# Kernel optimization log

Hardware: AMD Instinct MI355X
Metric: run time of the kernel (lower is better)

## Reference

```python
import jax, jax.numpy as jnp
import numpy as np


def setup_inputs() -> dict:
    key = jax.random.key(0)
    ks = jax.random.split(key, 8)
    N, D, E, R = 300000, 64, 1000000, 100000
    all_emb = jax.random.normal(ks[0], (N, D), jnp.float32)
    # xavier-ish init for the edge MLP (Linear(2D->D), Linear(D->1))
    W1 = jax.random.normal(ks[1], (D, 2 * D), jnp.float32) / np.sqrt(2.0 * D).astype(np.float32)
    b1 = jnp.zeros((D,), jnp.float32)
    W2 = jax.random.normal(ks[2], (1, D), jnp.float32) / np.sqrt(1.0 * D).astype(np.float32)
    b2 = jnp.zeros((1,), jnp.float32)
    edge_index = jax.random.randint(ks[3], (2, E), 0, N, jnp.int32)
    rand_idx = jax.random.randint(ks[4], (2, R), 0, N, jnp.int32)
    eps_u = jax.random.uniform(ks[5], (E, 1), jnp.float32)
    rb_u = jax.random.uniform(ks[6], (E,), jnp.float32)
    return dict(all_emb=all_emb, W1=W1, b1=b1, W2=W2, b2=b2,
                edge_index=edge_index, rand_idx=rand_idx, eps_u=eps_u, rb_u=rb_u)


def reference(all_emb, W1, b1, W2, b2, edge_index, rand_idx, eps_u, rb_u):
    src, dst = edge_index[0], edge_index[1]
    # gather + concat: [E, 2D]
    edge_emb = jnp.concatenate([all_emb[src], all_emb[dst]], axis=1)
    h = jax.nn.relu(edge_emb @ W1.T + b1)            # [E, D]
    edge_logits = h @ W2.T + b2                      # [E, 1]
    # Gumbel-sigmoid gate, temperature 1.0; eps ~ U(bias, 1-bias)
    bias = 1e-4
    eps = (bias - (1.0 - bias)) * eps_u + (1.0 - bias)
    gate = jnp.log(eps) - jnp.log1p(-eps) + edge_logits
    edge_weight = jax.nn.sigmoid(gate)[:, 0]         # [E]
    # __build_prob_neighbourhood: RelaxedBernoulli(temp=0.9, probs=clamp(w,.01,.99)).rsample()
    att = jnp.clip(edge_weight, 0.01, 0.99)
    u = jnp.clip(rb_u, 1e-7, 1.0 - 1e-7)
    t = 0.9
    sample = jax.nn.sigmoid((jnp.log(att) - jnp.log1p(-att) + jnp.log(u) - jnp.log1p(-u)) / t)
    mask = jax.lax.stop_gradient((sample > 0.0).astype(sample.dtype))
    mat = sample * mask
    # sparse rebuild: (edge_index, mat) + graph_random (rand_idx, 0.05), then coalesce
    rand_vals = jnp.full((rand_idx.shape[1],), 0.05, mat.dtype)
    rows = jnp.concatenate([src, rand_idx[0]])
    cols = jnp.concatenate([dst, rand_idx[1]])
    vals = jnp.concatenate([mat, rand_vals])
    order = jnp.lexsort((cols, rows))                # sort by (row, col)
    rows_s, cols_s, vals_s = rows[order], cols[order], vals[order]
    change = jnp.concatenate([jnp.ones((1,), bool),
                              (rows_s[1:] != rows_s[:-1]) | (cols_s[1:] != cols_s[:-1])])
    seg = jnp.cumsum(change) - 1                     # run id per sorted entry
    sums = jax.ops.segment_sum(vals_s, seg, num_segments=vals.shape[0])
    # coalesced value placed at first occurrence of each unique (row,col); dups zeroed
    out_vals = jnp.where(change, sums[seg], 0.0)
    return rows_s, cols_s, out_vals
```

## Files before the change

kernel.cpp:

```cpp
#include <hip/hip_runtime.h>
#include <stdint.h>

typedef unsigned short u16;
typedef unsigned int   u32;
typedef __attribute__((ext_vector_type(8))) short bf16x8;
typedef __attribute__((ext_vector_type(4))) float f32x4;

#define RSTRIDE 32

__device__ __forceinline__ float bflo(u32 u){ return __uint_as_float(u << 16); }
__device__ __forceinline__ u32 f2bf(float f){
  u32 u = __float_as_uint(f);
  return (u + 0x7fffu + ((u >> 16) & 1u)) >> 16;
}
__device__ __forceinline__ float qbf(float f){ return __uint_as_float(f2bf(f) << 16); }
__device__ __forceinline__ float decp(u32 p){
  u32 lo = p & 8191u;
  return __uint_as_float((lo ? lo + 8192u : 0u) << 16);
}

__global__ void k_zero(int* __restrict__ c, int N){
  int i = blockIdx.x * 256 + threadIdx.x;
  if (i < N) c[i] = 0;
}

__global__ void __launch_bounds__(256) k_mlp_fused(
    const u16* __restrict__ emb, const u16* __restrict__ W1,
    const u16* __restrict__ b1, const u16* __restrict__ W2,
    const u16* __restrict__ b2,
    const int* __restrict__ src, const int* __restrict__ dst,
    const u16* __restrict__ eps_u, const u16* __restrict__ rb_u,
    const int* __restrict__ rand0, const int* __restrict__ rand1,
    int* __restrict__ cnt, u32* __restrict__ packed,
    int E, int R, int ntp)
{
  int lane = threadIdx.x & 63;
  int c    = lane & 15;
  int quad = lane >> 4;
  int wid  = blockIdx.x * 4 + (threadIdx.x >> 6);
  int wstride = gridDim.x * 4;

  {
    int gtid = blockIdx.x * 256 + threadIdx.x;
    int gsz  = gridDim.x * 256;
    for (int i = gtid; i < R; i += gsz){
      int row = rand0[i];
      int rk = atomicAdd(&cnt[row], 1);
      if (rk < RSTRIDE)
        packed[(size_t)row * RSTRIDE + rk] = ((u32)rand1[i] << 13) | 7501u;
    }
  }

  bf16x8 bfr[4][4];
  #pragma unroll
  for (int ks = 0; ks < 4; ks++)
    #pragma unroll
    for (int t = 0; t < 4; t++)
      bfr[ks][t] = *(const bf16x8*)(W1 + (size_t)(t*16 + c)*128 + ks*32 + quad*8);

  float b1v[4], w2v[4];
  #pragma unroll
  for (int t = 0; t < 4; t++){
    b1v[t] = bflo((u32)b1[t*16 + c]);
    w2v[t] = bflo((u32)W2[t*16 + c]);
  }
  float b2v = bflo((u32)b2[0]);

  int nd = 0;
  if (wid < ntp){
    int idx = wid * 32 + (lane & 31);
    if (idx >= E) idx = E - 1;
    nd = (lane < 32) ? src[idx] : dst[idx];
  }

  for (int tp = wid; tp < ntp; tp += wstride){
    int e_base = tp * 32;

    int tpn = tp + wstride;
    int ndn = 0;
    if (tpn < ntp){
      int idxn = tpn * 32 + (lane & 31);
      if (idxn >= E) idxn = E - 1;
      ndn = (lane < 32) ? src[idxn] : dst[idxn];
    }

    int s0 = __shfl(nd, c),      d0 = __shfl(nd, 32 + c);
    int s1 = __shfl(nd, 16 + c), d1 = __shfl(nd, 48 + c);

    int tile = c >> 2, r = c & 3;
    int eo32 = tile * 16 + quad * 4 + r;
    int e_o  = e_base + eo32;
    bool act = (c < 8) && (e_o < E);
    int s_e = __shfl(nd, eo32);
    int d_e = __shfl(nd, 32 + eo32);

    int rk = 0;
    if (act) rk = atomicAdd(&cnt[s_e], 1);

    bf16x8 a0[4], a1[4];
    #pragma unroll
    for (int ks = 0; ks < 4; ks++){
      a0[ks] = *(const bf16x8*)(emb + (size_t)(ks < 2 ? s0 : d0) * 64 + (ks & 1) * 32 + quad * 8);
      a1[ks] = *(const bf16x8*)(emb + (size_t)(ks < 2 ? s1 : d1) * 64 + (ks & 1) * 32 + quad * 8);
    }

    float ue = 0.f, uu_raw = 0.f;
    if (act){
      ue     = bflo((u32)eps_u[e_o]);
      uu_raw = bflo((u32)rb_u[e_o]);
    }

    f32x4 acc0[4], acc1[4];
    #pragma unroll
    for (int t = 0; t < 4; t++){
      acc0[t] = (f32x4){0.f,0.f,0.f,0.f};
      acc1[t] = (f32x4){0.f,0.f,0.f,0.f};
    }
    #pragma unroll
    for (int ks = 0; ks < 4; ks++){
      #pragma unroll
      for (int t = 0; t < 4; t++){
        acc0[t] = __builtin_amdgcn_mfma_f32_16x16x32_bf16(a0[ks], bfr[ks][t], acc0[t], 0, 0, 0);
        acc1[t] = __builtin_amdgcn_mfma_f32_16x16x32_bf16(a1[ks], bfr[ks][t], acc1[t], 0, 0, 0);
      }
    }

    float pr0[4], pr1[4];
    #pragma unroll
    for (int rr = 0; rr < 4; rr++){
      float h0 = fmaxf(acc0[0][rr] + b1v[0], 0.f);
      float h1 = fmaxf(acc0[1][rr] + b1v[1], 0.f);
      float h2 = fmaxf(acc0[2][rr] + b1v[2], 0.f);
      float h3 = fmaxf(acc0[3][rr] + b1v[3], 0.f);
      pr0[rr] = h0*w2v[0] + h1*w2v[1] + h2*w2v[2] + h3*w2v[3];
      float g0 = fmaxf(acc1[0][rr] + b1v[0], 0.f);
      float g1 = fmaxf(acc1[1][rr] + b1v[1], 0.f);
      float g2 = fmaxf(acc1[2][rr] + b1v[2], 0.f);
      float g3 = fmaxf(acc1[3][rr] + b1v[3], 0.f);
      pr1[rr] = g0*w2v[0] + g1*w2v[1] + g2*w2v[2] + g3*w2v[3];
    }
    #pragma unroll
    for (int d = 1; d < 16; d <<= 1){
      #pragma unroll
      for (int rr = 0; rr < 4; rr++){
        pr0[rr] += __shfl_xor(pr0[rr], d);
        pr1[rr] += __shfl_xor(pr1[rr], d);
      }
    }

    if (act){
      float pv0 = (r==0)?pr0[0]:(r==1)?pr0[1]:(r==2)?pr0[2]:pr0[3];
      float pv1 = (r==0)?pr1[0]:(r==1)?pr1[1]:(r==2)?pr1[2]:pr1[3];
      float logit = (tile ? pv1 : pv0) + b2v;
      float eps = fmaf(-0.9998f, ue, 0.9999f);
      float gate = (__log2f(eps) - __log2f(1.0f - eps)) * 0.69314718f + logit;
      gate = fminf(fmaxf(gate, -4.59511985f), 4.59511985f);
      float uu = fminf(fmaxf(uu_raw, 1e-7f), 1.0f - 1e-7f);
      float lu = (__log2f(uu) - __log2f(1.0f - uu)) * 0.69314718f;
      float l  = (gate + lu) * (1.0f / 0.9f);
      float ee = __builtin_amdgcn_exp2f(-l * 1.44269504f);
      float val = 1.0f / (1.0f + ee);
      u32 h = f2bf(val);
      u32 code = (h >= 8192u) ? (h - 8192u) : 0u;
      if (rk < RSTRIDE)
        packed[(size_t)s_e * RSTRIDE + rk] = ((u32)d_e << 13) | code;
    }

    nd = ndn;
  }
}

__global__ void k_scan1(const int* __restrict__ cnt, int* __restrict__ rowstart,
                        int* __restrict__ bsum, int N){
  __shared__ int sh[256];
  int blk = blockIdx.x, tid = threadIdx.x;
  int base = blk * 1024 + tid * 4;
  int v0 = (base + 0 < N) ? min(cnt[base + 0], RSTRIDE) : 0;
  int v1 = (base + 1 < N) ? min(cnt[base + 1], RSTRIDE) : 0;
  int v2 = (base + 2 < N) ? min(cnt[base + 2], RSTRIDE) : 0;
  int v3 = (base + 3 < N) ? min(cnt[base + 3], RSTRIDE) : 0;
  int tot = v0 + v1 + v2 + v3;
  sh[tid] = tot;
  __syncthreads();
  for (int off = 1; off < 256; off <<= 1){
    int t2 = (tid >= off) ? sh[tid - off] : 0;
    __syncthreads();
    sh[tid] += t2;
    __syncthreads();
  }
  int excl = sh[tid] - tot;
  if (base + 0 < N) rowstart[base + 0] = excl;
  if (base + 1 < N) rowstart[base + 1] = excl + v0;
  if (base + 2 < N) rowstart[base + 2] = excl + v0 + v1;
  if (base + 3 < N) rowstart[base + 3] = excl + v0 + v1 + v2;
  if (tid == 255) bsum[blk] = sh[255];
}

__global__ void k_scan2(const int* __restrict__ bsum, int* __restrict__ boff, int NB){
  __shared__ int sh[512];
  int tid = threadIdx.x;
  int v = (tid < NB) ? bsum[tid] : 0;
  sh[tid] = v;
  __syncthreads();
  for (int off = 1; off < 512; off <<= 1){
    int t2 = (tid >= off) ? sh[tid - off] : 0;
    __syncthreads();
    sh[tid] += t2;
    __syncthreads();
  }
  boff[tid] = sh[tid] - v;
}

#define CAS(a,b) { u32 x = v[a], y = v[b]; v[a] = min(x,y); v[b] = max(x,y); }

__global__ void __launch_bounds__(256) k_emit(
    const int* __restrict__ rowstart, const int* __restrict__ boff,
    const int* __restrict__ cnt, u32* __restrict__ packed,
    float* __restrict__ out, int N, int M){
  int r = blockIdx.x * 256 + threadIdx.x;
  if (r >= N) return;
  int deg = min(cnt[r], RSTRIDE);
  int b = rowstart[r] + boff[r >> 10];
  float rf = qbf((float)r);

  if (deg <= 16){
    const uint4* seg4 = (const uint4*)(packed + (size_t)r * RSTRIDE);
    uint4 q0 = seg4[0], q1 = seg4[1], q2 = seg4[2], q3 = seg4[3];
    u32 v[16];
    v[0]=q0.x; v[1]=q0.y; v[2]=q0.z; v[3]=q0.w;
    v[4]=q1.x; v[5]=q1.y; v[6]=q1.z; v[7]=q1.w;
    v[8]=q2.x; v[9]=q2.y; v[10]=q2.z; v[11]=q2.w;
    v[12]=q3.x; v[13]=q3.y; v[14]=q3.z; v[15]=q3.w;
    #pragma unroll
    for (int i = 0; i < 16; i++) if (i >= deg) v[i] = 0xFFFFFFFFu;

    CAS(0,1) CAS(2,3) CAS(4,5) CAS(6,7) CAS(8,9) CAS(10,11) CAS(12,13) CAS(14,15)
    CAS(0,2) CAS(1,3) CAS(4,6) CAS(5,7) CAS(8,10) CAS(9,11) CAS(12,14) CAS(13,15)
    CAS(1,2) CAS(5,6) CAS(9,10) CAS(13,14)
    CAS(0,4) CAS(1,5) CAS(2,6) CAS(3,7) CAS(8,12) CAS(9,13) CAS(10,14) CAS(11,15)
    CAS(2,4) CAS(3,5) CAS(10,12) CAS(11,13)
    CAS(1,2) CAS(3,4) CAS(5,6) CAS(9,10) CAS(11,12) CAS(13,14)
    CAS(0,8) CAS(1,9) CAS(2,10) CAS(3,11) CAS(4,12) CAS(5,13) CAS(6,14) CAS(7,15)
    CAS(4,8) CAS(5,9) CAS(6,10) CAS(7,11)
    CAS(2,4) CAS(3,5) CAS(6,8) CAS(7,9) CAS(10,12) CAS(11,13)
    CAS(1,2) CAS(3,4) CAS(5,6) CAS(7,8) CAS(9,10) CAS(11,12) CAS(13,14)

    #pragma unroll
    for (int i = 0; i < 16; i++){
      if (i < deg){
        u32 coli = v[i] >> 13;
        bool head = (i == 0) || ((v[i-1] >> 13) != coli);
        float s = decp(v[i]);
        bool run = true;
        #pragma unroll
        for (int j = i + 1; j < 16; j++){
          run = run && (j < deg) && ((v[j] >> 13) == coli);
          if (run) s += decp(v[j]);
        }
        float cf = qbf((float)coli);
        out[b + i]         = rf;
        out[M + b + i]     = cf;
        out[2 * M + b + i] = head ? qbf(s) : 0.f;
      }
    }
    return;
  }

  u32* seg = packed + (size_t)r * RSTRIDE;
  for (int i = 1; i < deg; i++){
    u32 p = seg[i];
    int j = i - 1;
    while (j >= 0 && seg[j] > p){ seg[j+1] = seg[j]; j--; }
    seg[j+1] = p;
  }
  int i = 0;
  while (i < deg){
    u32 p = seg[i];
    u32 col = p >> 13;
    float sum = decp(p);
    int j = i + 1;
    while (j < deg && (seg[j] >> 13) == col){
      sum += decp(seg[j]);
      j++;
    }
    float cf = qbf((float)col);
    out[b + i] = rf; out[M + b + i] = cf; out[2 * M + b + i] = qbf(sum);
    for (int q = i + 1; q < j; q++){
      out[b + q] = rf; out[M + b + q] = cf; out[2 * M + b + q] = 0.f;
    }
    i = j;
  }
}

extern "C" void kernel_launch(void* const* d_in, const int* in_sizes, int n_in,
                              void* d_out, int out_size, void* d_ws, size_t ws_size,
                              hipStream_t stream){
  (void)n_in; (void)out_size; (void)ws_size;
  const u16* all_emb = (const u16*)d_in[0];
  const u16* W1   = (const u16*)d_in[1];
  const u16* b1   = (const u16*)d_in[2];
  const u16* W2   = (const u16*)d_in[3];
  const u16* b2   = (const u16*)d_in[4];
  const int* edge_index = (const int*)d_in[5];
  const int* rand_idx   = (const int*)d_in[6];
  const u16* eps_u = (const u16*)d_in[7];
  const u16* rb_u  = (const u16*)d_in[8];

  int N = in_sizes[0] / 64;
  int E = in_sizes[5] / 2;
  int R = in_sizes[6] / 2;
  int M = E + R;
  const int* src   = edge_index;
  const int* dst   = edge_index + E;
  const int* rand0 = rand_idx;
  const int* rand1 = rand_idx + R;

  int* cnt      = (int*)d_ws;
  int* rowstart = cnt + N;
  int* bsum     = rowstart + N;
  int* boff     = bsum + 512;
  u32* packed   = (u32*)(boff + 512);

  k_zero<<<(N + 255) / 256, 256, 0, stream>>>(cnt, N);
  int ntp = (E + 31) / 32;
  k_mlp_fused<<<2048, 256, 0, stream>>>(all_emb, W1, b1, W2, b2, src, dst,
                                        eps_u, rb_u, rand0, rand1,
                                        cnt, packed, E, R, ntp);
  int NB = (N + 1023) / 1024;
  k_scan1<<<NB, 256, 0, stream>>>(cnt, rowstart, bsum, N);
  k_scan2<<<1, 512, 0, stream>>>(bsum, boff, NB);
  k_emit<<<(N + 255) / 256, 256, 0, stream>>>(rowstart, boff, cnt, packed,
                                              (float*)d_out, N, M);
}
```

Before: 239.3 us.

## Replace three-kernel scan with block-sum kernel and in-emit prefix computation

Removes the two-level scan kernels (k_scan1, k_scan2) and the rowstart array. A small kernel now computes per-256-row block sums, and k_emit derives its block offset by reducing all preceding block sums, then does an intra-block scan to get each row's start. This drops one kernel launch and the rowstart write/read, at the cost of each emit block redundantly summing up to ~1200 preceding block sums plus added synchronisation inside k_emit. It also adds an early return for rows with zero degree.

```diff
diff --git a/kernel.cpp b/kernel.cpp
--- a/kernel.cpp
+++ b/kernel.cpp
@@ -170,17 +170,46 @@
   }
 }
 
-__global__ void k_scan1(const int* __restrict__ cnt, int* __restrict__ rowstart,
-                        int* __restrict__ bsum, int N){
+__global__ void __launch_bounds__(256) k_bsum(
+    const int* __restrict__ cnt, int* __restrict__ bsum, int N){
   __shared__ int sh[256];
-  int blk = blockIdx.x, tid = threadIdx.x;
-  int base = blk * 1024 + tid * 4;
-  int v0 = (base + 0 < N) ? min(cnt[base + 0], RSTRIDE) : 0;
-  int v1 = (base + 1 < N) ? min(cnt[base + 1], RSTRIDE) : 0;
-  int v2 = (base + 2 < N) ? min(cnt[base + 2], RSTRIDE) : 0;
-  int v3 = (base + 3 < N) ? min(cnt[base + 3], RSTRIDE) : 0;
-  int tot = v0 + v1 + v2 + v3;
-  sh[tid] = tot;
+  int tid = threadIdx.x;
+  int r = blockIdx.x * 256 + tid;
+  sh[tid] = (r < N) ? min(cnt[r], RSTRIDE) : 0;
+  __syncthreads();
+  #pragma unroll
+  for (int off = 128; off > 0; off >>= 1){
+    if (tid < off) sh[tid] += sh[tid + off];
+    __syncthreads();
+  }
+  if (tid == 0) bsum[blockIdx.x] = sh[0];
+}
+
+#define CAS(a,b) { u32 x = v[a], y = v[b]; v[a] = min(x,y); v[b] = max(x,y); }
+
+__global__ void __launch_bounds__(256) k_emit(
+    const int* __restrict__ cnt, const int* __restrict__ bsum,
+    u32* __restrict__ packed, float* __restrict__ out,
+    int N, int M, int NSB){
+  __shared__ int sh[256];
+  int tid = threadIdx.x;
+  int blk = blockIdx.x;
+  int r = blk * 256 + tid;
+  int deg = (r < N) ? min(cnt[r], RSTRIDE) : 0;
+
+  int part = 0;
+  for (int i = tid; i < blk; i += 256) part += bsum[i];
+  sh[tid] = part;
+  __syncthreads();
+  #pragma unroll
+  for (int off = 128; off > 0; off >>= 1){
+    if (tid < off) sh[tid] += sh[tid + off];
+    __syncthreads();
+  }
+  int base = sh[0];
+  __syncthreads();
+
+  sh[tid] = deg;
   __syncthreads();
   for (int off = 1; off < 256; off <<= 1){
     int t2 = (tid >= off) ? sh[tid - off] : 0;
@@ -188,39 +217,9 @@
     sh[tid] += t2;
     __syncthreads();
   }
-  int excl = sh[tid] - tot;
-  if (base + 0 < N) rowstart[base + 0] = excl;
-  if (base + 1 < N) rowstart[base + 1] = excl + v0;
-  if (base + 2 < N) rowstart[base + 2] = excl + v0 + v1;
-  if (base + 3 < N) rowstart[base + 3] = excl + v0 + v1 + v2;
-  if (tid == 255) bsum[blk] = sh[255];
-}
-
-__global__ void k_scan2(const int* __restrict__ bsum, int* __restrict__ boff, int NB){
-  __shared__ int sh[512];
-  int tid = threadIdx.x;
-  int v = (tid < NB) ? bsum[tid] : 0;
-  sh[tid] = v;
-  __syncthreads();
-  for (int off = 1; off < 512; off <<= 1){
-    int t2 = (tid >= off) ? sh[tid - off] : 0;
-    __syncthreads();
-    sh[tid] += t2;
-    __syncthreads();
-  }
-  boff[tid] = sh[tid] - v;
-}
-
-#define CAS(a,b) { u32 x = v[a], y = v[b]; v[a] = min(x,y); v[b] = max(x,y); }
-
-__global__ void __launch_bounds__(256) k_emit(
-    const int* __restrict__ rowstart, const int* __restrict__ boff,
-    const int* __restrict__ cnt, u32* __restrict__ packed,
-    float* __restrict__ out, int N, int M){
-  int r = blockIdx.x * 256 + threadIdx.x;
-  if (r >= N) return;
-  int deg = min(cnt[r], RSTRIDE);
-  int b = rowstart[r] + boff[r >> 10];
+  int b = base + sh[tid] - deg;
+
+  if (r >= N || deg == 0) return;
   float rf = qbf((float)r);
 
   if (deg <= 16){
@@ -315,20 +314,16 @@
   const int* rand0 = rand_idx;
   const int* rand1 = rand_idx + R;
 
-  int* cnt      = (int*)d_ws;
-  int* rowstart = cnt + N;
-  int* bsum     = rowstart + N;
-  int* boff     = bsum + 512;
-  u32* packed   = (u32*)(boff + 512);
-
+  int* cnt    = (int*)d_ws;
+  int* bsum   = cnt + N;
+  u32* packed = (u32*)(bsum + 2048);
+
+  int NSB = (N + 255) / 256;
   k_zero<<<(N + 255) / 256, 256, 0, stream>>>(cnt, N);
   int ntp = (E + 31) / 32;
   k_mlp_fused<<<2048, 256, 0, stream>>>(all_emb, W1, b1, W2, b2, src, dst,
                                         eps_u, rb_u, rand0, rand1,
                                         cnt, packed, E, R, ntp);
-  int NB = (N + 1023) / 1024;
-  k_scan1<<<NB, 256, 0, stream>>>(cnt, rowstart, bsum, N);
-  k_scan2<<<1, 512, 0, stream>>>(bsum, boff, NB);
-  k_emit<<<(N + 255) / 256, 256, 0, stream>>>(rowstart, boff, cnt, packed,
-                                              (float*)d_out, N, M);
-}
+  k_bsum<<<NSB, 256, 0, stream>>>(cnt, bsum, N);
+  k_emit<<<NSB, 256, 0, stream>>>(cnt, bsum, packed, (float*)d_out, N, M, NSB);
+}
```

Measured after the change: 236.9 us. About the same (-1.0%).
